# Kernel tuning notes

Hardware: AMD Instinct MI355X
Metric: run time of the kernel (lower is better)

## Reference

```python
import jax, jax.numpy as jnp
import numpy as np

B, T, D = 2, 2048, 1024
H, DK, DV = 16, 64, 64
FF = 4096
EPS = 1e-6


def layer_norm(x, gamma, beta):
    mu = jnp.mean(x, axis=-1, keepdims=True)
    var = jnp.var(x, axis=-1, keepdims=True)
    return (x - mu) * jax.lax.rsqrt(var + EPS) * gamma + beta


def setup_inputs() -> dict:
    key = jax.random.key(0)
    ks = jax.random.split(key, 16)
    s = 0.02
    return {
        "inputs": jax.random.normal(ks[0], (B, T, D), jnp.float32),
        "Wq": jax.random.normal(ks[1], (D, H, DK), jnp.float32) * s,
        "Wk": jax.random.normal(ks[2], (D, H, DK), jnp.float32) * s,
        "Wv": jax.random.normal(ks[3], (D, H, DV), jnp.float32) * s,
        "Wo": jax.random.normal(ks[4], (D, H, DV), jnp.float32) * s,
        "W1": jax.random.normal(ks[5], (D, FF), jnp.float32) * s,
        "b1": jnp.zeros((FF,), jnp.float32),
        "W2": jax.random.normal(ks[6], (FF, D), jnp.float32) * s,
        "b2": jnp.zeros((D,), jnp.float32),
        "g1": jnp.ones((D,), jnp.float32),
        "be1": jnp.zeros((D,), jnp.float32),
        "g2": jnp.ones((D,), jnp.float32),
        "be2": jnp.zeros((D,), jnp.float32),
    }


def reference(inputs, Wq, Wk, Wv, Wo, W1, b1, W2, b2, g1, be1, g2, be2):
    x = inputs
    scale = 1.0 / jnp.sqrt(jnp.asarray(DK, x.dtype))
    q = jnp.einsum("btd,dhk->bthk", x, Wq) * scale
    k = jnp.einsum("bsd,dhk->bshk", x, Wk)
    v = jnp.einsum("bsd,dhv->bshv", x, Wv)
    # [B,H,T,S] attention scores; causal mask (t >= s)
    score = jnp.einsum("bshk,bthk->bhts", k, q)
    causal = jnp.tril(jnp.ones((T, T), bool))  # [T,S]
    score = jnp.where(causal[None, None], score, jnp.finfo(score.dtype).min)
    attn = jax.nn.softmax(score, axis=-1)
    ctx = jnp.einsum("bhts,bshv->bthv", attn, v)
    attn_out = jnp.einsum("bthv,dhv->btd", ctx, Wo)
    h = layer_norm(x + attn_out, g1, be1)
    ffn = jnp.maximum(h @ W1 + b1, 0.0) @ W2 + b2
    return layer_norm(h + ffn, g2, be2)
```

## Files before the change

kernel.cpp:

```cpp
#include <hip/hip_runtime.h>
#include <math.h>

#define T_SEQ 2048
#define D_MODEL 1024
#define NHEAD 16
#define DHEAD 64
#define FF_DIM 4096
#define NTOK 4096
#define LN_EPS 1e-6f

typedef unsigned short u16;
typedef unsigned int u32;
typedef __attribute__((ext_vector_type(8))) __bf16 bf16x8;
typedef __attribute__((ext_vector_type(4))) float f32x4;
typedef __attribute__((ext_vector_type(16))) float f32x16;

typedef const void __attribute__((address_space(1))) gvoid;
typedef void __attribute__((address_space(3))) lvoid;

__device__ __forceinline__ u16 f2bf(float f) {
  unsigned u = __float_as_uint(f);
  return (u16)((u + 0x7fffu + ((u >> 16) & 1u)) >> 16);
}
__device__ __forceinline__ float bf2f(u16 u) {
  return __uint_as_float((unsigned)u << 16);
}
__device__ __forceinline__ u32 cvtpk(float lo, float hi) {
  u32 r;
  asm("v_cvt_pk_bf16_f32 %0, %1, %2" : "=v"(r) : "v"(lo), "v"(hi));
  return r;
}

__device__ __forceinline__ void gll16(const u16* g, u16* l) {
  __builtin_amdgcn_global_load_lds((gvoid*)g, (lvoid*)l, 16, 0, 0);
}

__device__ __forceinline__ bf16x8 lds_frag(const u16* lds, int row, int chunk) {
  return *(const bf16x8*)&lds[row * 64 + ((chunk ^ (row & 7)) * 8)];
}

union BF8 { u32 u[4]; bf16x8 v; };

__global__ __launch_bounds__(256) void conv_f2b(const float* __restrict__ in,
                                                u16* __restrict__ out, int n) {
  const int i = (blockIdx.x * 256 + threadIdx.x) * 4;
  if (i >= n) return;
  const float4 v = *(const float4*)&in[i];
  ushort4 o;
  o.x = f2bf(v.x); o.y = f2bf(v.y); o.z = f2bf(v.z); o.w = f2bf(v.w);
  *(ushort4*)&out[i] = o;
}

__global__ __launch_bounds__(256) void transpose_f2b(
    const float* __restrict__ in, u16* __restrict__ out, int K, int N,
    float scale) {
  __shared__ u16 t[64][72];
  const int tid = threadIdx.x;
  const int k0 = blockIdx.y * 64, n0 = blockIdx.x * 64;
  const int nl = tid & 63;
#pragma unroll
  for (int i = 0; i < 16; ++i) {
    const int kl = (tid >> 6) * 16 + i;
    t[nl][kl] = f2bf(in[(size_t)(k0 + kl) * N + n0 + nl] * scale);
  }
  __syncthreads();
  const int nr = tid >> 2, kc = (tid & 3) * 16;
  const uint4 a = *(const uint4*)&t[nr][kc];
  const uint4 b = *(const uint4*)&t[nr][kc + 8];
  *(uint4*)&out[(size_t)(n0 + nr) * K + k0 + kc] = a;
  *(uint4*)&out[(size_t)(n0 + nr) * K + k0 + kc + 8] = b;
}

__global__ __launch_bounds__(256) void transpose_v(const u16* __restrict__ vin,
                                                   u16* __restrict__ vout) {
  __shared__ u16 t[64][72];
  const int tid = threadIdx.x;
  const int bh = blockIdx.y;
  const int t0 = blockIdx.x * 64;
  const u16* src = vin + ((size_t)bh * T_SEQ + t0) * 64;
#pragma unroll
  for (int i = 0; i < 2; ++i) {
    const int r = i * 32 + (tid >> 3);
    const int ch = tid & 7;
    *(uint4*)&t[r][ch * 8] = *(const uint4*)&src[(size_t)r * 64 + ch * 8];
  }
  __syncthreads();
  const int d = tid >> 2, p = (tid & 3) * 16;
  alignas(16) u16 tmp[16];
#pragma unroll
  for (int i = 0; i < 16; ++i) tmp[i] = t[p + i][d];
  u16* dst = vout + ((size_t)bh * 64 + d) * T_SEQ + t0 + p;
  *(uint4*)&dst[0] = *(const uint4*)&tmp[0];
  *(uint4*)&dst[8] = *(const uint4*)&tmp[8];
}

template <int OUTMODE, bool BIAS, bool RELU>
__global__ __launch_bounds__(256) void gemm_mfma(
    const u16* __restrict__ A, const u16* __restrict__ BT,
    const float* __restrict__ bias, void* __restrict__ C,
    int M, int N, int K, float scale) {
  __shared__ u16 smem[16384];

  const int tid = threadIdx.x;
  const int w = tid >> 6, lane = tid & 63;

  const int nwg = gridDim.x * gridDim.y;
  int bid = blockIdx.y * gridDim.x + blockIdx.x;
  const int cpx = nwg >> 3;
  bid = (bid & 7) * cpx + (bid >> 3);
  const int bx = bid % gridDim.x, by = bid / gridDim.x;
  const int m0 = by * 128, n0 = bx * 128;
  const int wr = (w >> 1) * 64, wc = (w & 1) * 64;

  f32x4 acc[4][4];
#pragma unroll
  for (int i = 0; i < 4; ++i)
#pragma unroll
    for (int j = 0; j < 4; ++j) acc[i][j] = (f32x4)0.f;

  const int srow = w * 32 + (lane >> 2);
  const int scol = (lane & 3) * 8;
  const u16* gA0 = A + (size_t)(m0 + srow) * K + scol;
  const u16* gA1 = gA0 + (size_t)16 * K;
  const u16* gB0 = BT + (size_t)(n0 + srow) * K + scol;
  const u16* gB1 = gB0 + (size_t)16 * K;

  const int arow = lane & 15;
  const int koff = (lane >> 4) * 8;

  auto stage = [&](int buf, int k0) {
    u16* base = smem + buf * 8192;
    gll16(gA0 + k0, base + w * 1024);
    gll16(gA1 + k0, base + w * 1024 + 512);
    gll16(gB0 + k0, base + 4096 + w * 1024);
    gll16(gB1 + k0, base + 4096 + w * 1024 + 512);
  };

  stage(0, 0);
  __syncthreads();

  const int nk = K >> 5;
  for (int it = 0; it < nk; ++it) {
    const int buf = it & 1;
    if (it + 1 < nk) stage(buf ^ 1, (it + 1) << 5);

    const u16* sb = smem + buf * 8192;
    bf16x8 af[4], bff[4];
#pragma unroll
    for (int m = 0; m < 4; ++m)
      af[m] = *(const bf16x8*)&sb[(wr + m * 16 + arow) * 32 + koff];
#pragma unroll
    for (int n = 0; n < 4; ++n)
      bff[n] = *(const bf16x8*)&sb[4096 + (wc + n * 16 + arow) * 32 + koff];
#pragma unroll
    for (int m = 0; m < 4; ++m)
#pragma unroll
      for (int n = 0; n < 4; ++n)
        acc[m][n] = __builtin_amdgcn_mfma_f32_16x16x32_bf16(
            af[m], bff[n], acc[m][n], 0, 0, 0);
    __syncthreads();
  }

  const int rbase = (lane >> 4) * 4;
  const int cl = lane & 15;
#pragma unroll
  for (int n = 0; n < 4; ++n) {
    const int col = n0 + wc + n * 16 + cl;
    const float bia = BIAS ? bias[col] : 0.f;
#pragma unroll
    for (int m = 0; m < 4; ++m) {
      const int row0 = m0 + wr + m * 16 + rbase;
#pragma unroll
      for (int r = 0; r < 4; ++r) {
        float vv = acc[m][n][r] * scale + bia;
        if (RELU) vv = fmaxf(vv, 0.f);
        const int row = row0 + r;
        if (OUTMODE == 1) {
          ((u16*)C)[(size_t)row * N + col] = f2bf(vv);
        } else {
          const int reg = col >> 10, cl2 = col & 1023;
          const size_t off =
              (size_t)reg * 4194304 +
              ((size_t)((row >> 11) * NHEAD + (cl2 >> 6)) * T_SEQ +
               (row & 2047)) * 64 + (cl2 & 63);
          ((u16*)C)[off] = f2bf(vv);
        }
      }
    }
  }
}

__global__ __launch_bounds__(256) void attn_mfma(
    const u16* __restrict__ qg, const u16* __restrict__ kg,
    const u16* __restrict__ vtg, u16* __restrict__ ctx) {
  __shared__ u16 Ks[2][64 * 64];
  __shared__ u16 Vs[2][64 * 64];

  const int tid = threadIdx.x;
  const int w = tid >> 6, lane = tid & 63;
  const int qt = gridDim.x - 1 - blockIdx.x;
  const int bh = blockIdx.y;
  const int l31 = lane & 31, hi32 = lane >> 5;
  const int r8 = lane >> 3, cswz = (lane & 7) ^ r8;

  const u16* qhead = qg + (size_t)bh * (T_SEQ * 64);
  const u16* khead = kg + (size_t)bh * (T_SEQ * 64);
  const u16* vhead = vtg + (size_t)bh * (64 * T_SEQ);

  const int qbase = qt * 128;
  const int qrow = qbase + w * 32 + l31;

  bf16x8 qb[4];
#pragma unroll
  for (int ks2 = 0; ks2 < 4; ++ks2)
    qb[ks2] = *(const bf16x8*)&qhead[(size_t)qrow * 64 + ks2 * 16 + hi32 * 8];

  f32x16 o0 = (f32x16)0.f, o1 = (f32x16)0.f;
  float m = -INFINITY, l = 0.f;

  const int nt = 2 * qt + 2;

  auto stage = [&](int buf, int s0) {
#pragma unroll
    for (int i = 0; i < 2; ++i) {
      const int row = w * 16 + i * 8 + r8;
      gll16(khead + (size_t)(s0 + row) * 64 + cswz * 8,
            &Ks[buf][(w * 16 + i * 8) * 64]);
      gll16(vhead + (size_t)row * T_SEQ + s0 + cswz * 8,
            &Vs[buf][(w * 16 + i * 8) * 64]);
    }
  };

  stage(0, 0);
  __syncthreads();

  for (int it = 0; it < nt; ++it) {
    const int buf = it & 1;
    if (it + 1 < nt) stage(buf ^ 1, (it + 1) * 64);

    const bool lastT = (it == nt - 1), diagT = (it == nt - 2);
    if (!(lastT && w < 2)) {
      f32x16 st0 = (f32x16)0.f, st1 = (f32x16)0.f;
      __builtin_amdgcn_s_setprio(1);
#pragma unroll
      for (int ks2 = 0; ks2 < 4; ++ks2) {
        const bf16x8 kf0 = lds_frag(Ks[buf], l31, ks2 * 2 + hi32);
        st0 = __builtin_amdgcn_mfma_f32_32x32x16_bf16(kf0, qb[ks2], st0, 0, 0, 0);
      }
#pragma unroll
      for (int ks2 = 0; ks2 < 4; ++ks2) {
        const bf16x8 kf1 = lds_frag(Ks[buf], 32 + l31, ks2 * 2 + hi32);
        st1 = __builtin_amdgcn_mfma_f32_32x32x16_bf16(kf1, qb[ks2], st1, 0, 0, 0);
      }
      __builtin_amdgcn_s_setprio(0);

      if ((diagT && w < 2) || (lastT && w >= 2)) {
        const int s0g = it * 64;
#pragma unroll
        for (int r = 0; r < 16; ++r) {
          const int rowm = (r & 3) + 8 * (r >> 2) + 4 * hi32;
          if (s0g + rowm > qrow) st0[r] = -1e30f;
          if (s0g + 32 + rowm > qrow) st1[r] = -1e30f;
        }
      }

      float mx = fmaxf(st0[0], st1[0]);
#pragma unroll
      for (int r = 1; r < 16; ++r) mx = fmaxf(mx, fmaxf(st0[r], st1[r]));
      mx = fmaxf(mx, __shfl_xor(mx, 32));

      float corr = 1.f;
      if (!__all(mx <= m + 11.5f)) {
        const float mn = fmaxf(m, mx);
        corr = exp2f(m - mn);
        m = mn;
#pragma unroll
        for (int r = 0; r < 16; ++r) { o0[r] *= corr; o1[r] *= corr; }
      }
      float ps = 0.f;
#pragma unroll
      for (int r = 0; r < 16; ++r) {
        st0[r] = exp2f(st0[r] - m);
        st1[r] = exp2f(st1[r] - m);
        ps += st0[r] + st1[r];
      }
      ps += __shfl_xor(ps, 32);
      l = l * corr + ps;

      BF8 pb[4];
#pragma unroll
      for (int blk = 0; blk < 2; ++blk) {
        {
          u32 x0 = cvtpk(st0[blk * 8 + 0], st0[blk * 8 + 1]);
          u32 x1 = cvtpk(st0[blk * 8 + 2], st0[blk * 8 + 3]);
          u32 y0 = cvtpk(st0[blk * 8 + 4], st0[blk * 8 + 5]);
          u32 y1 = cvtpk(st0[blk * 8 + 6], st0[blk * 8 + 7]);
          asm("v_permlane32_swap_b32 %0, %1" : "+v"(x0), "+v"(y0));
          asm("v_permlane32_swap_b32 %0, %1" : "+v"(x1), "+v"(y1));
          pb[blk].u[0] = x0; pb[blk].u[1] = x1;
          pb[blk].u[2] = y0; pb[blk].u[3] = y1;
        }
        {
          u32 x0 = cvtpk(st1[blk * 8 + 0], st1[blk * 8 + 1]);
          u32 x1 = cvtpk(st1[blk * 8 + 2], st1[blk * 8 + 3]);
          u32 y0 = cvtpk(st1[blk * 8 + 4], st1[blk * 8 + 5]);
          u32 y1 = cvtpk(st1[blk * 8 + 6], st1[blk * 8 + 7]);
          asm("v_permlane32_swap_b32 %0, %1" : "+v"(x0), "+v"(y0));
          asm("v_permlane32_swap_b32 %0, %1" : "+v"(x1), "+v"(y1));
          pb[2 + blk].u[0] = x0; pb[2 + blk].u[1] = x1;
          pb[2 + blk].u[2] = y0; pb[2 + blk].u[3] = y1;
        }
      }

      __builtin_amdgcn_s_setprio(1);
#pragma unroll
      for (int ks = 0; ks < 4; ++ks) {
        const bf16x8 vf0 = lds_frag(Vs[buf], l31, ks * 2 + hi32);
        o0 = __builtin_amdgcn_mfma_f32_32x32x16_bf16(vf0, pb[ks].v, o0, 0, 0, 0);
      }
#pragma unroll
      for (int ks = 0; ks < 4; ++ks) {
        const bf16x8 vf1 = lds_frag(Vs[buf], 32 + l31, ks * 2 + hi32);
        o1 = __builtin_amdgcn_mfma_f32_32x32x16_bf16(vf1, pb[ks].v, o1, 0, 0, 0);
      }
      __builtin_amdgcn_s_setprio(0);
    }
    __syncthreads();
  }

  const float inv = 1.0f / l;
#pragma unroll
  for (int r = 0; r < 16; ++r) { o0[r] *= inv; o1[r] *= inv; }

  u16* ep = &Ks[0][0] + w * 2048;
#pragma unroll
  for (int rg = 0; rg < 4; ++rg) {
    const u32 w0 = cvtpk(o0[rg * 4 + 0], o0[rg * 4 + 1]);
    const u32 w1 = cvtpk(o0[rg * 4 + 2], o0[rg * 4 + 3]);
    uint2 val; val.x = w0; val.y = w1;
    *(uint2*)&ep[l31 * 64 + ((rg ^ (l31 & 7)) * 8) + hi32 * 4] = val;
  }
#pragma unroll
  for (int rg = 0; rg < 4; ++rg) {
    const u32 w0 = cvtpk(o1[rg * 4 + 0], o1[rg * 4 + 1]);
    const u32 w1 = cvtpk(o1[rg * 4 + 2], o1[rg * 4 + 3]);
    const int chunk = 4 + rg;
    uint2 val; val.x = w0; val.y = w1;
    *(uint2*)&ep[l31 * 64 + ((chunk ^ (l31 & 7)) * 8) + hi32 * 4] = val;
  }

  const int b = bh >> 4, h = bh & 15;
  const int ql = lane >> 1, half = lane & 1;
  const int t = qbase + w * 32 + ql;
  u16* dst = ctx + ((size_t)(b * T_SEQ + t) * NHEAD + h) * 64;
#pragma unroll
  for (int j = 0; j < 4; ++j) {
    const int chunk = half * 4 + j;
    const uint4 vv = *(const uint4*)&ep[ql * 64 + ((chunk ^ (ql & 7)) * 8)];
    *(uint4*)&dst[chunk * 8] = vv;
  }
}

template <bool EMIT_BF>
__global__ __launch_bounds__(256) void add_layernorm(
    const float* __restrict__ x, const u16* __restrict__ y,
    const float* __restrict__ g, const float* __restrict__ be,
    float* __restrict__ out, u16* __restrict__ out_bf) {
  const int row = blockIdx.x;
  const int tid = threadIdx.x;
  const size_t base = (size_t)row * D_MODEL + tid * 4;

  const float4 xv = *(const float4*)&x[base];
  const ushort4 yv = *(const ushort4*)&y[base];
  const float v0 = xv.x + bf2f(yv.x), v1 = xv.y + bf2f(yv.y);
  const float v2 = xv.z + bf2f(yv.z), v3 = xv.w + bf2f(yv.w);

  float s = v0 + v1 + v2 + v3;
  float ss = v0 * v0 + v1 * v1 + v2 * v2 + v3 * v3;
#pragma unroll
  for (int off = 32; off > 0; off >>= 1) {
    s += __shfl_down(s, off);
    ss += __shfl_down(ss, off);
  }
  __shared__ float red[8];
  const int wid = tid >> 6, lane = tid & 63;
  if (lane == 0) { red[wid] = s; red[4 + wid] = ss; }
  __syncthreads();
  s = red[0] + red[1] + red[2] + red[3];
  ss = red[4] + red[5] + red[6] + red[7];

  const float mean = s * (1.0f / D_MODEL);
  const float var = ss * (1.0f / D_MODEL) - mean * mean;
  const float rr = rsqrtf(var + LN_EPS);

  const float4 g4 = *(const float4*)&g[tid * 4];
  const float4 b4 = *(const float4*)&be[tid * 4];
  float4 o4;
  o4.x = (v0 - mean) * rr * g4.x + b4.x;
  o4.y = (v1 - mean) * rr * g4.y + b4.y;
  o4.z = (v2 - mean) * rr * g4.z + b4.z;
  o4.w = (v3 - mean) * rr * g4.w + b4.w;
  *(float4*)&out[base] = o4;
  if (EMIT_BF) {
    ushort4 ob;
    ob.x = f2bf(o4.x); ob.y = f2bf(o4.y); ob.z = f2bf(o4.z); ob.w = f2bf(o4.w);
    *(ushort4*)&out_bf[base] = ob;
  }
}

extern "C" void kernel_launch(void* const* d_in, const int* in_sizes, int n_in,
                              void* d_out, int out_size, void* d_ws,
                              size_t ws_size, hipStream_t stream) {
  const float* x  = (const float*)d_in[0];
  const float* Wq = (const float*)d_in[1];
  const float* Wk = (const float*)d_in[2];
  const float* Wv = (const float*)d_in[3];
  const float* Wo = (const float*)d_in[4];
  const float* W1 = (const float*)d_in[5];
  const float* b1 = (const float*)d_in[6];
  const float* W2 = (const float*)d_in[7];
  const float* b2 = (const float*)d_in[8];
  const float* g1 = (const float*)d_in[9];
  const float* be1 = (const float*)d_in[10];
  const float* g2 = (const float*)d_in[11];
  const float* be2 = (const float*)d_in[12];

  char* ws = (char*)d_ws;
  const size_t MB = 1u << 20;
  u16*   x_bf    = (u16*)(ws + 0 * MB);
  u16*   WqkvT   = (u16*)(ws + 8 * MB);
  u16*   WoB     = (u16*)(ws + 14 * MB);
  u16*   W1T     = (u16*)(ws + 16 * MB);
  u16*   W2T     = (u16*)(ws + 24 * MB);
  u16*   q_bf    = (u16*)(ws + 32 * MB);
  u16*   v_bf    = (u16*)(ws + 48 * MB);
  u16*   vT_bf   = (u16*)(ws + 56 * MB);
  u16*   ctx_bf  = (u16*)(ws + 64 * MB);
  u16*   attn_bf = (u16*)(ws + 72 * MB);
  float* h       = (float*)(ws + 80 * MB);
  u16*   h_bf    = (u16*)(ws + 0 * MB);
  u16*   ffn1_bf = (u16*)(ws + 32 * MB);
  u16*   ffn2_bf = (u16*)(ws + 8 * MB);

  const dim3 blk(256);
  const float lg2e = 1.44269504f;

  conv_f2b<<<NTOK, blk, 0, stream>>>(x, x_bf, NTOK * D_MODEL);
  transpose_f2b<<<dim3(16, 16), blk, 0, stream>>>(Wq, WqkvT, D_MODEL, D_MODEL,
                                                  0.125f * lg2e);
  transpose_f2b<<<dim3(16, 16), blk, 0, stream>>>(Wk, WqkvT + 1024 * 1024,
                                                  D_MODEL, D_MODEL, 1.f);
  transpose_f2b<<<dim3(16, 16), blk, 0, stream>>>(Wv, WqkvT + 2 * 1024 * 1024,
                                                  D_MODEL, D_MODEL, 1.f);
  conv_f2b<<<1024, blk, 0, stream>>>(Wo, WoB, D_MODEL * D_MODEL);
  transpose_f2b<<<dim3(64, 16), blk, 0, stream>>>(W1, W1T, D_MODEL, FF_DIM, 1.f);
  transpose_f2b<<<dim3(16, 64), blk, 0, stream>>>(W2, W2T, FF_DIM, D_MODEL, 1.f);

  gemm_mfma<2, false, false><<<dim3(24, 32), blk, 0, stream>>>(
      x_bf, WqkvT, nullptr, q_bf, NTOK, 3072, D_MODEL, 1.f);

  transpose_v<<<dim3(32, 32), blk, 0, stream>>>(v_bf, vT_bf);

  attn_mfma<<<dim3(T_SEQ / 128, 32), blk, 0, stream>>>(q_bf, q_bf + 4194304,
                                                       vT_bf, ctx_bf);

  gemm_mfma<1, false, false><<<dim3(8, 32), blk, 0, stream>>>(
      ctx_bf, WoB, nullptr, attn_bf, NTOK, D_MODEL, D_MODEL, 1.f);

  add_layernorm<true><<<NTOK, blk, 0, stream>>>(x, attn_bf, g1, be1, h, h_bf);

  gemm_mfma<1, true, true><<<dim3(32, 32), blk, 0, stream>>>(
      h_bf, W1T, b1, ffn1_bf, NTOK, FF_DIM, D_MODEL, 1.f);
  gemm_mfma<1, true, false><<<dim3(8, 32), blk, 0, stream>>>(
      ffn1_bf, W2T, b2, ffn2_bf, NTOK, D_MODEL, FF_DIM, 1.f);

  add_layernorm<false><<<NTOK, blk, 0, stream>>>(h, ffn2_bf, g2, be2,
                                                 (float*)d_out, nullptr);
}
```

Baseline: 401.4 us.

## Split-K the N=1024 GEMMs and shrink attention blocks to 64 queries

```diff
diff --git a/kernel.cpp b/kernel.cpp
--- a/kernel.cpp
+++ b/kernel.cpp
@@ -94,7 +94,7 @@
   *(uint4*)&dst[8] = *(const uint4*)&tmp[8];
 }
 
-template <int OUTMODE, bool BIAS, bool RELU>
+template <int OUTMODE, bool BIAS, bool RELU, int SPLITK>
 __global__ __launch_bounds__(256) void gemm_mfma(
     const u16* __restrict__ A, const u16* __restrict__ BT,
     const float* __restrict__ bias, void* __restrict__ C,
@@ -112,6 +112,9 @@
   const int m0 = by * 128, n0 = bx * 128;
   const int wr = (w >> 1) * 64, wc = (w & 1) * 64;
 
+  const int kpb = K / SPLITK;
+  const int kbase = blockIdx.z * kpb;
+
   f32x4 acc[4][4];
 #pragma unroll
   for (int i = 0; i < 4; ++i)
@@ -120,9 +123,9 @@
 
   const int srow = w * 32 + (lane >> 2);
   const int scol = (lane & 3) * 8;
-  const u16* gA0 = A + (size_t)(m0 + srow) * K + scol;
+  const u16* gA0 = A + (size_t)(m0 + srow) * K + kbase + scol;
   const u16* gA1 = gA0 + (size_t)16 * K;
-  const u16* gB0 = BT + (size_t)(n0 + srow) * K + scol;
+  const u16* gB0 = BT + (size_t)(n0 + srow) * K + kbase + scol;
   const u16* gB1 = gB0 + (size_t)16 * K;
 
   const int arow = lane & 15;
@@ -139,7 +142,7 @@
   stage(0, 0);
   __syncthreads();
 
-  const int nk = K >> 5;
+  const int nk = kpb >> 5;
   for (int it = 0; it < nk; ++it) {
     const int buf = it & 1;
     if (it + 1 < nk) stage(buf ^ 1, (it + 1) << 5);
@@ -161,6 +164,8 @@
     __syncthreads();
   }
 
+  u16* Cb = (u16*)C;
+  if (SPLITK > 1) Cb += (size_t)blockIdx.z * M * N;
   const int rbase = (lane >> 4) * 4;
   const int cl = lane & 15;
 #pragma unroll
@@ -176,21 +181,21 @@
         if (RELU) vv = fmaxf(vv, 0.f);
         const int row = row0 + r;
         if (OUTMODE == 1) {
-          ((u16*)C)[(size_t)row * N + col] = f2bf(vv);
+          Cb[(size_t)row * N + col] = f2bf(vv);
         } else {
           const int reg = col >> 10, cl2 = col & 1023;
           const size_t off =
               (size_t)reg * 4194304 +
               ((size_t)((row >> 11) * NHEAD + (cl2 >> 6)) * T_SEQ +
                (row & 2047)) * 64 + (cl2 & 63);
-          ((u16*)C)[off] = f2bf(vv);
+          Cb[off] = f2bf(vv);
         }
       }
     }
   }
 }
 
-__global__ __launch_bounds__(256) void attn_mfma(
+__global__ __launch_bounds__(128) void attn_mfma(
     const u16* __restrict__ qg, const u16* __restrict__ kg,
     const u16* __restrict__ vtg, u16* __restrict__ ctx) {
   __shared__ u16 Ks[2][64 * 64];
@@ -207,7 +212,7 @@
   const u16* khead = kg + (size_t)bh * (T_SEQ * 64);
   const u16* vhead = vtg + (size_t)bh * (64 * T_SEQ);
 
-  const int qbase = qt * 128;
+  const int qbase = qt * 64;
   const int qrow = qbase + w * 32 + l31;
 
   bf16x8 qb[4];
@@ -218,16 +223,16 @@
   f32x16 o0 = (f32x16)0.f, o1 = (f32x16)0.f;
   float m = -INFINITY, l = 0.f;
 
-  const int nt = 2 * qt + 2;
+  const int nt = qt + 1;
 
   auto stage = [&](int buf, int s0) {
 #pragma unroll
-    for (int i = 0; i < 2; ++i) {
-      const int row = w * 16 + i * 8 + r8;
+    for (int i = 0; i < 4; ++i) {
+      const int row = w * 32 + i * 8 + r8;
       gll16(khead + (size_t)(s0 + row) * 64 + cswz * 8,
-            &Ks[buf][(w * 16 + i * 8) * 64]);
+            &Ks[buf][(w * 32 + i * 8) * 64]);
       gll16(vhead + (size_t)row * T_SEQ + s0 + cswz * 8,
-            &Vs[buf][(w * 16 + i * 8) * 64]);
+            &Vs[buf][(w * 32 + i * 8) * 64]);
     }
   };
 
@@ -238,93 +243,90 @@
     const int buf = it & 1;
     if (it + 1 < nt) stage(buf ^ 1, (it + 1) * 64);
 
-    const bool lastT = (it == nt - 1), diagT = (it == nt - 2);
-    if (!(lastT && w < 2)) {
-      f32x16 st0 = (f32x16)0.f, st1 = (f32x16)0.f;
-      __builtin_amdgcn_s_setprio(1);
-#pragma unroll
-      for (int ks2 = 0; ks2 < 4; ++ks2) {
-        const bf16x8 kf0 = lds_frag(Ks[buf], l31, ks2 * 2 + hi32);
-        st0 = __builtin_amdgcn_mfma_f32_32x32x16_bf16(kf0, qb[ks2], st0, 0, 0, 0);
+    f32x16 st0 = (f32x16)0.f, st1 = (f32x16)0.f;
+    __builtin_amdgcn_s_setprio(1);
+#pragma unroll
+    for (int ks2 = 0; ks2 < 4; ++ks2) {
+      const bf16x8 kf0 = lds_frag(Ks[buf], l31, ks2 * 2 + hi32);
+      st0 = __builtin_amdgcn_mfma_f32_32x32x16_bf16(kf0, qb[ks2], st0, 0, 0, 0);
+    }
+#pragma unroll
+    for (int ks2 = 0; ks2 < 4; ++ks2) {
+      const bf16x8 kf1 = lds_frag(Ks[buf], 32 + l31, ks2 * 2 + hi32);
+      st1 = __builtin_amdgcn_mfma_f32_32x32x16_bf16(kf1, qb[ks2], st1, 0, 0, 0);
+    }
+    __builtin_amdgcn_s_setprio(0);
+
+    if (it == nt - 1) {
+      const int s0g = it * 64;
+#pragma unroll
+      for (int r = 0; r < 16; ++r) {
+        const int rowm = (r & 3) + 8 * (r >> 2) + 4 * hi32;
+        if (s0g + rowm > qrow) st0[r] = -1e30f;
+        if (s0g + 32 + rowm > qrow) st1[r] = -1e30f;
       }
-#pragma unroll
-      for (int ks2 = 0; ks2 < 4; ++ks2) {
-        const bf16x8 kf1 = lds_frag(Ks[buf], 32 + l31, ks2 * 2 + hi32);
-        st1 = __builtin_amdgcn_mfma_f32_32x32x16_bf16(kf1, qb[ks2], st1, 0, 0, 0);
+    }
+
+    float mx = fmaxf(st0[0], st1[0]);
+#pragma unroll
+    for (int r = 1; r < 16; ++r) mx = fmaxf(mx, fmaxf(st0[r], st1[r]));
+    mx = fmaxf(mx, __shfl_xor(mx, 32));
+
+    float corr = 1.f;
+    if (!__all(mx <= m + 11.5f)) {
+      const float mn = fmaxf(m, mx);
+      corr = exp2f(m - mn);
+      m = mn;
+#pragma unroll
+      for (int r = 0; r < 16; ++r) { o0[r] *= corr; o1[r] *= corr; }
+    }
+    float ps = 0.f;
+#pragma unroll
+    for (int r = 0; r < 16; ++r) {
+      st0[r] = exp2f(st0[r] - m);
+      st1[r] = exp2f(st1[r] - m);
+      ps += st0[r] + st1[r];
+    }
+    ps += __shfl_xor(ps, 32);
+    l = l * corr + ps;
+
+    BF8 pb[4];
+#pragma unroll
+    for (int blk = 0; blk < 2; ++blk) {
+      {
+        u32 x0 = cvtpk(st0[blk * 8 + 0], st0[blk * 8 + 1]);
+        u32 x1 = cvtpk(st0[blk * 8 + 2], st0[blk * 8 + 3]);
+        u32 y0 = cvtpk(st0[blk * 8 + 4], st0[blk * 8 + 5]);
+        u32 y1 = cvtpk(st0[blk * 8 + 6], st0[blk * 8 + 7]);
+        asm("v_permlane32_swap_b32 %0, %1" : "+v"(x0), "+v"(y0));
+        asm("v_permlane32_swap_b32 %0, %1" : "+v"(x1), "+v"(y1));
+        pb[blk].u[0] = x0; pb[blk].u[1] = x1;
+        pb[blk].u[2] = y0; pb[blk].u[3] = y1;
       }
-      __builtin_amdgcn_s_setprio(0);
-
-      if ((diagT && w < 2) || (lastT && w >= 2)) {
-        const int s0g = it * 64;
-#pragma unroll
-        for (int r = 0; r < 16; ++r) {
-          const int rowm = (r & 3) + 8 * (r >> 2) + 4 * hi32;
-          if (s0g + rowm > qrow) st0[r] = -1e30f;
-          if (s0g + 32 + rowm > qrow) st1[r] = -1e30f;
-        }
+      {
+        u32 x0 = cvtpk(st1[blk * 8 + 0], st1[blk * 8 + 1]);
+        u32 x1 = cvtpk(st1[blk * 8 + 2], st1[blk * 8 + 3]);
+        u32 y0 = cvtpk(st1[blk * 8 + 4], st1[blk * 8 + 5]);
+        u32 y1 = cvtpk(st1[blk * 8 + 6], st1[blk * 8 + 7]);
+        asm("v_permlane32_swap_b32 %0, %1" : "+v"(x0), "+v"(y0));
+        asm("v_permlane32_swap_b32 %0, %1" : "+v"(x1), "+v"(y1));
+        pb[2 + blk].u[0] = x0; pb[2 + blk].u[1] = x1;
+        pb[2 + blk].u[2] = y0; pb[2 + blk].u[3] = y1;
       }
-
-      float mx = fmaxf(st0[0], st1[0]);
-#pragma unroll
-      for (int r = 1; r < 16; ++r) mx = fmaxf(mx, fmaxf(st0[r], st1[r]));
-      mx = fmaxf(mx, __shfl_xor(mx, 32));
-
-      float corr = 1.f;
-      if (!__all(mx <= m + 11.5f)) {
-        const float mn = fmaxf(m, mx);
-        corr = exp2f(m - mn);
-        m = mn;
-#pragma unroll
-        for (int r = 0; r < 16; ++r) { o0[r] *= corr; o1[r] *= corr; }
-      }
-      float ps = 0.f;
-#pragma unroll
-      for (int r = 0; r < 16; ++r) {
-        st0[r] = exp2f(st0[r] - m);
-        st1[r] = exp2f(st1[r] - m);
-        ps += st0[r] + st1[r];
-      }
-      ps += __shfl_xor(ps, 32);
-      l = l * corr + ps;
-
-      BF8 pb[4];
-#pragma unroll
-      for (int blk = 0; blk < 2; ++blk) {
-        {
-          u32 x0 = cvtpk(st0[blk * 8 + 0], st0[blk * 8 + 1]);
-          u32 x1 = cvtpk(st0[blk * 8 + 2], st0[blk * 8 + 3]);
-          u32 y0 = cvtpk(st0[blk * 8 + 4], st0[blk * 8 + 5]);
-          u32 y1 = cvtpk(st0[blk * 8 + 6], st0[blk * 8 + 7]);
-          asm("v_permlane32_swap_b32 %0, %1" : "+v"(x0), "+v"(y0));
-          asm("v_permlane32_swap_b32 %0, %1" : "+v"(x1), "+v"(y1));
-          pb[blk].u[0] = x0; pb[blk].u[1] = x1;
-          pb[blk].u[2] = y0; pb[blk].u[3] = y1;
-        }
-        {
-          u32 x0 = cvtpk(st1[blk * 8 + 0], st1[blk * 8 + 1]);
-          u32 x1 = cvtpk(st1[blk * 8 + 2], st1[blk * 8 + 3]);
-          u32 y0 = cvtpk(st1[blk * 8 + 4], st1[blk * 8 + 5]);
-          u32 y1 = cvtpk(st1[blk * 8 + 6], st1[blk * 8 + 7]);
-          asm("v_permlane32_swap_b32 %0, %1" : "+v"(x0), "+v"(y0));
-          asm("v_permlane32_swap_b32 %0, %1" : "+v"(x1), "+v"(y1));
-          pb[2 + blk].u[0] = x0; pb[2 + blk].u[1] = x1;
-          pb[2 + blk].u[2] = y0; pb[2 + blk].u[3] = y1;
-        }
-      }
-
-      __builtin_amdgcn_s_setprio(1);
-#pragma unroll
-      for (int ks = 0; ks < 4; ++ks) {
-        const bf16x8 vf0 = lds_frag(Vs[buf], l31, ks * 2 + hi32);
-        o0 = __builtin_amdgcn_mfma_f32_32x32x16_bf16(vf0, pb[ks].v, o0, 0, 0, 0);
-      }
-#pragma unroll
-      for (int ks = 0; ks < 4; ++ks) {
-        const bf16x8 vf1 = lds_frag(Vs[buf], 32 + l31, ks * 2 + hi32);
-        o1 = __builtin_amdgcn_mfma_f32_32x32x16_bf16(vf1, pb[ks].v, o1, 0, 0, 0);
-      }
-      __builtin_amdgcn_s_setprio(0);
-    }
+    }
+
+    __builtin_amdgcn_s_setprio(1);
+#pragma unroll
+    for (int ks = 0; ks < 4; ++ks) {
+      const bf16x8 vf0 = lds_frag(Vs[buf], l31, ks * 2 + hi32);
+      o0 = __builtin_amdgcn_mfma_f32_32x32x16_bf16(vf0, pb[ks].v, o0, 0, 0, 0);
+    }
+#pragma unroll
+    for (int ks = 0; ks < 4; ++ks) {
+      const bf16x8 vf1 = lds_frag(Vs[buf], 32 + l31, ks * 2 + hi32);
+      o1 = __builtin_amdgcn_mfma_f32_32x32x16_bf16(vf1, pb[ks].v, o1, 0, 0, 0);
+    }
+    __builtin_amdgcn_s_setprio(0);
     __syncthreads();
   }
 
@@ -363,7 +365,8 @@
 
 template <bool EMIT_BF>
 __global__ __launch_bounds__(256) void add_layernorm(
-    const float* __restrict__ x, const u16* __restrict__ y,
+    const float* __restrict__ x, const u16* __restrict__ y0,
+    const u16* __restrict__ y1, const float* __restrict__ bias,
     const float* __restrict__ g, const float* __restrict__ be,
     float* __restrict__ out, u16* __restrict__ out_bf) {
   const int row = blockIdx.x;
@@ -371,9 +374,18 @@
   const size_t base = (size_t)row * D_MODEL + tid * 4;
 
   const float4 xv = *(const float4*)&x[base];
-  const ushort4 yv = *(const ushort4*)&y[base];
-  const float v0 = xv.x + bf2f(yv.x), v1 = xv.y + bf2f(yv.y);
-  const float v2 = xv.z + bf2f(yv.z), v3 = xv.w + bf2f(yv.w);
+  const ushort4 y0v = *(const ushort4*)&y0[base];
+  float v0 = xv.x + bf2f(y0v.x), v1 = xv.y + bf2f(y0v.y);
+  float v2 = xv.z + bf2f(y0v.z), v3 = xv.w + bf2f(y0v.w);
+  if (y1) {
+    const ushort4 y1v = *(const ushort4*)&y1[base];
+    v0 += bf2f(y1v.x); v1 += bf2f(y1v.y);
+    v2 += bf2f(y1v.z); v3 += bf2f(y1v.w);
+  }
+  if (bias) {
+    const float4 bv = *(const float4*)&bias[tid * 4];
+    v0 += bv.x; v1 += bv.y; v2 += bv.z; v3 += bv.w;
+  }
 
   float s = v0 + v1 + v2 + v3;
   float ss = v0 * v0 + v1 * v1 + v2 * v2 + v3 * v3;
@@ -436,11 +448,11 @@
   u16*   v_bf    = (u16*)(ws + 48 * MB);
   u16*   vT_bf   = (u16*)(ws + 56 * MB);
   u16*   ctx_bf  = (u16*)(ws + 64 * MB);
-  u16*   attn_bf = (u16*)(ws + 72 * MB);
+  u16*   attn01  = (u16*)(ws + 32 * MB);
   float* h       = (float*)(ws + 80 * MB);
   u16*   h_bf    = (u16*)(ws + 0 * MB);
   u16*   ffn1_bf = (u16*)(ws + 32 * MB);
-  u16*   ffn2_bf = (u16*)(ws + 8 * MB);
+  u16*   ffn2_01 = (u16*)(ws + 64 * MB);
 
   const dim3 blk(256);
   const float lg2e = 1.44269504f;
@@ -456,24 +468,26 @@
   transpose_f2b<<<dim3(64, 16), blk, 0, stream>>>(W1, W1T, D_MODEL, FF_DIM, 1.f);
   transpose_f2b<<<dim3(16, 64), blk, 0, stream>>>(W2, W2T, FF_DIM, D_MODEL, 1.f);
 
-  gemm_mfma<2, false, false><<<dim3(24, 32), blk, 0, stream>>>(
+  gemm_mfma<2, false, false, 1><<<dim3(24, 32), blk, 0, stream>>>(
       x_bf, WqkvT, nullptr, q_bf, NTOK, 3072, D_MODEL, 1.f);
 
   transpose_v<<<dim3(32, 32), blk, 0, stream>>>(v_bf, vT_bf);
 
-  attn_mfma<<<dim3(T_SEQ / 128, 32), blk, 0, stream>>>(q_bf, q_bf + 4194304,
-                                                       vT_bf, ctx_bf);
-
-  gemm_mfma<1, false, false><<<dim3(8, 32), blk, 0, stream>>>(
-      ctx_bf, WoB, nullptr, attn_bf, NTOK, D_MODEL, D_MODEL, 1.f);
-
-  add_layernorm<true><<<NTOK, blk, 0, stream>>>(x, attn_bf, g1, be1, h, h_bf);
-
-  gemm_mfma<1, true, true><<<dim3(32, 32), blk, 0, stream>>>(
+  attn_mfma<<<dim3(T_SEQ / 64, 32), dim3(128), 0, stream>>>(
+      q_bf, q_bf + 4194304, vT_bf, ctx_bf);
+
+  gemm_mfma<1, false, false, 2><<<dim3(8, 32, 2), blk, 0, stream>>>(
+      ctx_bf, WoB, nullptr, attn01, NTOK, D_MODEL, D_MODEL, 1.f);
+
+  add_layernorm<true><<<NTOK, blk, 0, stream>>>(
+      x, attn01, attn01 + 4194304, nullptr, g1, be1, h, h_bf);
+
+  gemm_mfma<1, true, true, 1><<<dim3(32, 32), blk, 0, stream>>>(
       h_bf, W1T, b1, ffn1_bf, NTOK, FF_DIM, D_MODEL, 1.f);
-  gemm_mfma<1, true, false><<<dim3(8, 32), blk, 0, stream>>>(
-      ffn1_bf, W2T, b2, ffn2_bf, NTOK, D_MODEL, FF_DIM, 1.f);
-
-  add_layernorm<false><<<NTOK, blk, 0, stream>>>(h, ffn2_bf, g2, be2,
-                                                 (float*)d_out, nullptr);
-}
+
+  gemm_mfma<1, false, false, 2><<<dim3(8, 32, 2), blk, 0, stream>>>(
+      ffn1_bf, W2T, nullptr, ffn2_01, NTOK, D_MODEL, FF_DIM, 1.f);
+
+  add_layernorm<false><<<NTOK, blk, 0, stream>>>(
+      h, ffn2_01, ffn2_01 + 4194304, b2, g2, be2, (float*)d_out, nullptr);
+}
```

Measured after the change: 386.1 us. 1.04x faster.
